# Kernel tuning notes

Measured on AMD Instinct MI355X. Metric: run time of the kernel, lower is better.

The kernel has to match this reference:

```python
import jax, jax.numpy as jnp
import numpy as np

T = 0.07          # temperature
K_POS = 5         # top-k positives per noun and for mask prediction
MARGIN = 0.1
LAM_CONTRAST = 0.6
LAM_MASK = 0.4


def _l2n(x):
    return x / jnp.linalg.norm(x, axis=-1, keepdims=True)


def setup_inputs() -> dict:
    key = jax.random.key(0)
    k0, k1, k2, k3 = jax.random.split(key, 4)
    B, N, D, M = 64, 576, 512, 16  # N = 24*24 patch grid
    patch_feats = _l2n(jax.random.normal(k0, (B, N, D), jnp.float32))
    noun_feats = _l2n(jax.random.normal(k1, (B, M, D), jnp.float32))
    global_img_feat = _l2n(jax.random.normal(k2, (B, D), jnp.float32))
    global_txt_feat = _l2n(jax.random.normal(k3, (B, D), jnp.float32))
    logit_scale = jnp.full((1,), 1.0 / 0.07, jnp.float32)
    idx = jnp.arange(B, dtype=jnp.int32)
    return {
        "patch_feats": patch_feats,
        "noun_feats": noun_feats,
        "global_img_feat": global_img_feat,
        "global_txt_feat": global_txt_feat,
        "logit_scale": logit_scale,
        "idx": idx,
    }


def _fine_grained_loss(patch_feats, noun_feats):
    # sim[b,m,n] = <noun_m, patch_n>; replaces the nested Python loops.
    B = patch_feats.shape[0]
    sim = jnp.einsum('bmd,bnd->bmn', noun_feats, patch_feats)
    scaled = sim / T
    # Per-noun contrastive loss. log_softmax over cat([topk, rest]) equals
    # log_softmax over all N entries evaluated at the topk positions, so:
    #   loss = -sum_topk log_softmax = K_POS*lse - sum(topk scaled values)
    lse = jax.nn.logsumexp(scaled, axis=-1)              # [B, M]
    topv, _ = jax.lax.top_k(scaled, K_POS)               # [B, M, K]
    contrast_loss = jnp.mean(K_POS * lse - topv.sum(-1))
    # Mask-prediction BCE loss (pool_type='mean').
    pooled = sim.mean(axis=1)                            # [B, N]
    _, tidx = jax.lax.top_k(pooled, K_POS)               # [B, K]
    pred = jnp.zeros_like(pooled).at[jnp.arange(B)[:, None], tidx].set(1.0)
    x = pooled / T
    mask_loss = jnp.mean(jnp.logaddexp(0.0, x) - x * pred)
    return LAM_CONTRAST * contrast_loss + LAM_MASK * mask_loss


def _contrastive_loss(img, txt, logit_scale, idx):
    logits = logit_scale.reshape(()) * (img @ txt.T)
    pos = (idx[:, None] == idx[None, :]).astype(logits.dtype)
    labels = pos / pos.sum(axis=1, keepdims=True)
    li2t = -(jax.nn.log_softmax(logits, axis=1) * labels).sum(1).mean()
    lt2i = -(jax.nn.log_softmax(logits.T, axis=1) * labels).sum(1).mean()
    return 0.5 * (li2t + lt2i)


def _triplet_loss(img, txt):
    scores = img @ txt.T
    d = jnp.diagonal(scores)
    eye = jnp.eye(scores.shape[0], dtype=bool)
    cost_s = jnp.where(eye, 0.0, jnp.clip(MARGIN + scores - d[:, None], 0.0)).sum()
    cost_im = jnp.where(eye, 0.0, jnp.clip(MARGIN + scores - d[None, :], 0.0)).sum()
    return 0.5 * (cost_s + cost_im)


def reference(patch_feats, noun_feats, global_img_feat, global_txt_feat, logit_scale, idx):
    loss_c = _contrastive_loss(global_img_feat, global_txt_feat, logit_scale, idx)
    loss_t = _triplet_loss(global_img_feat, global_txt_feat)
    loss_f = _fine_grained_loss(patch_feats, noun_feats)
    return jnp.stack([loss_c, loss_t, loss_f])
```

## Files before the change

### kernel.cpp

```cpp
#include <hip/hip_runtime.h>
#include <hip/hip_bf16.h>
#include <math.h>

#define NB 64
#define NN 576
#define ND 512
#define NM 16
#define QPB 9
#define KPOS 5
#define TINV 14.2857142857142857f

#define NFINE (NB * QPB)
#define NBLK1 (NFINE + NB)
#define WS_SIM 4096

#define FINF __builtin_inff()

typedef __attribute__((ext_vector_type(8))) short short8;
typedef __attribute__((ext_vector_type(4))) float floatx4;

__device__ __forceinline__ short f2bf(float f) {
  unsigned u = __float_as_uint(f);
  u += 0x7FFFu + ((u >> 16) & 1u);
  return (short)(u >> 16);
}

__device__ __forceinline__ short8 pack8(const float4 a, const float4 b) {
  short8 r;
  r[0] = f2bf(a.x); r[1] = f2bf(a.y); r[2] = f2bf(a.z); r[3] = f2bf(a.w);
  r[4] = f2bf(b.x); r[5] = f2bf(b.y); r[6] = f2bf(b.z); r[7] = f2bf(b.w);
  return r;
}

__device__ __forceinline__ void ins5(float (&a)[5], float v) {
  if (v > a[4]) {
    a[4] = v;
    if (a[4] > a[3]) { float x = a[4]; a[4] = a[3]; a[3] = x; }
    if (a[3] > a[2]) { float x = a[3]; a[3] = a[2]; a[2] = x; }
    if (a[2] > a[1]) { float x = a[2]; a[2] = a[1]; a[1] = x; }
    if (a[1] > a[0]) { float x = a[1]; a[1] = a[0]; a[0] = x; }
  }
}

__device__ __forceinline__ void merge5(float (&a)[5], const float (&b)[5]) {
  float r[5];
#pragma unroll
  for (int k = 0; k < 5; ++k) {
    float best = -FINF;
#pragma unroll
    for (int i = 0; i <= k + 1; ++i) {
      const int j = k + 1 - i;
      const float av = (i == 0) ? FINF : a[i - 1];
      const float bv = (j == 0) ? FINF : b[j - 1];
      best = fmaxf(best, fminf(av, bv));
    }
    r[k] = best;
  }
#pragma unroll
  for (int k = 0; k < 5; ++k) a[k] = r[k];
}

__device__ __forceinline__ void merge5_shfl(float (&a)[5], int msk) {
  float o[5];
#pragma unroll
  for (int k = 0; k < 5; ++k) o[k] = __shfl_xor(a[k], msk, 64);
  merge5(a, o);
}

__global__ __launch_bounds__(256) void k_sim(
    const float* __restrict__ patch, const float* __restrict__ noun,
    const float* __restrict__ gimg, const float* __restrict__ gtxt,
    float* __restrict__ ws) {
  const int blk = blockIdx.x;
  const int t = threadIdx.x;
  const int lane = t & 63;

  __shared__ float L[256];

  if (blk < NFINE) {
    const int b = blk / QPB, quad = blk - b * QPB;
    const int w = t >> 6;
    const int nidx = lane & 15;
    const int k0 = (lane >> 4) * 8;

    const float* nrow = noun + ((size_t)b * NM + nidx) * ND + k0;
    const float* prow = patch + ((size_t)(b * NN + quad * 64 + w * 16 + nidx)) * ND + k0;

    floatx4 acc = {0.f, 0.f, 0.f, 0.f};
#pragma unroll
    for (int ks = 0; ks < 16; ++ks) {
      const int o = ks * 32;
      const float4 a0 = *(const float4*)(nrow + o);
      const float4 a1 = *(const float4*)(nrow + o + 4);
      const float4 p0 = *(const float4*)(prow + o);
      const float4 p1 = *(const float4*)(prow + o + 4);
      const short8 af = pack8(a0, a1);
      const short8 bf = pack8(p0, p1);
      acc = __builtin_amdgcn_mfma_f32_16x16x32_bf16(af, bf, acc, 0, 0, 0);
    }

    float* dst = ws + WS_SIM + (size_t)blk * 1024;
    const int mrow = (lane >> 4) * 4;
    const int pcol = w * 16 + nidx;
#pragma unroll
    for (int r = 0; r < 4; ++r) dst[(mrow + r) * 64 + pcol] = acc[r];
  } else {
    const int i = blk - NFINE;
    const int dq = t >> 6;
    const float4* ip = (const float4*)(gimg + (size_t)i * ND + dq * 128);
    const float4* tp = (const float4*)(gtxt + (size_t)lane * ND + dq * 128);
    float a = 0.f;
#pragma unroll
    for (int q = 0; q < 32; ++q) {
      const float4 x = ip[q];
      const float4 y = tp[q];
      a += x.x * y.x + x.y * y.y + x.z * y.z + x.w * y.w;
    }
    L[dq * 64 + lane] = a;
    __syncthreads();
    if (t < 64) ws[i * 64 + t] = L[t] + L[64 + t] + L[128 + t] + L[192 + t];
  }
}

__global__ __launch_bounds__(256) void k_loss(
    const float* __restrict__ ws, const float* __restrict__ lscale,
    const int* __restrict__ idx, float* __restrict__ out) {
  const int blk = blockIdx.x;
  const int t = threadIdx.x;
  const int lane = t & 63;
  const int w = t >> 6;

  __shared__ float S[NM * 577 + 64];

  if (blk < NB) {
    const int b = blk;
#pragma unroll
    for (int q = 0; q < QPB; ++q) {
      const float4* t0 = (const float4*)(ws + WS_SIM + (size_t)(b * QPB + q) * 1024);
      const float4 a = t0[t];
      const int i0 = 4 * t;
      const int m = i0 >> 6, p = i0 & 63;
      float* dst = &S[m * 577 + q * 64 + p];
      dst[0] = a.x * TINV;
      dst[1] = a.y * TINV;
      dst[2] = a.z * TINV;
      dst[3] = a.w * TINV;
    }
    __syncthreads();

    float cpart = 0.f;
#pragma unroll
    for (int mi = 0; mi < 4; ++mi) {
      const int m = w * 4 + mi;
      const float* row = &S[m * 577];
      float mx = -FINF;
#pragma unroll
      for (int k = 0; k < 9; ++k) mx = fmaxf(mx, row[lane + 64 * k]);
#pragma unroll
      for (int msk = 1; msk < 64; msk <<= 1) mx = fmaxf(mx, __shfl_xor(mx, msk, 64));
      float se = 0.f;
      float t5[5] = {-FINF, -FINF, -FINF, -FINF, -FINF};
#pragma unroll
      for (int k = 0; k < 9; ++k) {
        const float v = row[lane + 64 * k];
        se += expf(v - mx);
        ins5(t5, v);
      }
#pragma unroll
      for (int msk = 1; msk < 64; msk <<= 1) {
        se += __shfl_xor(se, msk, 64);
        merge5_shfl(t5, msk);
      }
      if (lane == 0) {
        const float st = t5[0] + t5[1] + t5[2] + t5[3] + t5[4];
        cpart += (KPOS * (mx + logf(se)) - st) * (0.6f / (float)(NB * NM));
      }
    }

    float sxp = 0.f;
    float u5[5] = {-FINF, -FINF, -FINF, -FINF, -FINF};
#pragma unroll
    for (int rep = 0; rep < 3; ++rep) {
      const int n = t + rep * 256;
      if (n < NN) {
        float cs = 0.f;
#pragma unroll
        for (int m = 0; m < NM; ++m) cs += S[m * 577 + n];
        const float x = cs * (1.f / 16.f);
        sxp += (x > 0.f) ? (x + log1pf(expf(-x))) : log1pf(expf(x));
        ins5(u5, x);
      }
    }
#pragma unroll
    for (int msk = 1; msk < 64; msk <<= 1) {
      sxp += __shfl_xor(sxp, msk, 64);
      merge5_shfl(u5, msk);
    }
    float* R = &S[NM * 577];
    if (lane == 0) {
      R[w] = cpart;
      R[8 + w] = sxp;
#pragma unroll
      for (int k = 0; k < 5; ++k) R[16 + w * 5 + k] = u5[k];
    }
    __syncthreads();
    if (t == 0) {
      float tot = R[0] + R[1] + R[2] + R[3];
      float sp = R[8] + R[9] + R[10] + R[11];
      float f5[5] = {R[16], R[17], R[18], R[19], R[20]};
#pragma unroll
      for (int ww = 1; ww < 4; ++ww) {
        float o[5] = {R[16 + ww * 5], R[17 + ww * 5], R[18 + ww * 5],
                      R[19 + ww * 5], R[20 + ww * 5]};
        merge5(f5, o);
      }
      const float st = f5[0] + f5[1] + f5[2] + f5[3] + f5[4];
      tot += (sp - st) * (0.4f / (float)(NB * NN));
      atomicAdd(out + 2, tot);
    }
    return;
  }

  float* S_ = &S[0];
  for (int i = t; i < 4096; i += 256) S_[(i >> 6) * 65 + (i & 63)] = ws[i];
  __syncthreads();
  float* dgp = &S[4160];
  int* idl = (int*)&S[4224];
  if (t < 64) { dgp[t] = S_[t * 66]; idl[t] = idx[t]; }
  __syncthreads();
  if (t < 64) {
    const float sc = lscale[0];
    float mR = -FINF, mC = -FINF;
    for (int j = 0; j < 64; ++j) {
      mR = fmaxf(mR, sc * S_[t * 65 + j]);
      mC = fmaxf(mC, sc * S_[j * 65 + t]);
    }
    float seR = 0.f, seC = 0.f;
    for (int j = 0; j < 64; ++j) {
      seR += expf(sc * S_[t * 65 + j] - mR);
      seC += expf(sc * S_[j * 65 + t] - mC);
    }
    const float lseR = mR + logf(seR);
    const float lseC = mC + logf(seC);
    const int myid = idl[t];
    const float di = dgp[t];
    float ps = 0.f, trow = 0.f, tcol = 0.f, cs = 0.f, ci = 0.f;
    for (int j = 0; j < 64; ++j) {
      const float sv = S_[t * 65 + j];
      const float svT = S_[j * 65 + t];
      if (idl[j] == myid) {
        ps += 1.f;
        trow += sc * sv - lseR;
        tcol += sc * svT - lseC;
      }
      if (j != t) {
        cs += fmaxf(0.f, 0.1f + sv - di);
        ci += fmaxf(0.f, 0.1f + sv - dgp[j]);
      }
    }
    float vc = -(trow + tcol) / ps;
    float vt = cs + ci;
#pragma unroll
    for (int msk = 1; msk < 64; msk <<= 1) {
      vc += __shfl_xor(vc, msk, 64);
      vt += __shfl_xor(vt, msk, 64);
    }
    if (t == 0) {
      out[0] = vc * (0.5f / 64.f);
      out[1] = vt * 0.5f;
    }
  }
}

extern "C" void kernel_launch(void* const* d_in, const int* in_sizes, int n_in,
                              void* d_out, int out_size, void* d_ws, size_t ws_size,
                              hipStream_t stream) {
  const float* patch = (const float*)d_in[0];
  const float* noun  = (const float*)d_in[1];
  const float* gimg  = (const float*)d_in[2];
  const float* gtxt  = (const float*)d_in[3];
  const float* lsc   = (const float*)d_in[4];
  const int*   idx   = (const int*)d_in[5];
  float* out = (float*)d_out;
  float* ws  = (float*)d_ws;

  hipMemsetAsync(d_out, 0, 3 * sizeof(float), stream);
  k_sim<<<dim3(NBLK1), dim3(256), 0, stream>>>(patch, noun, gimg, gtxt, ws);
  k_loss<<<dim3(NB + 1), dim3(256), 0, stream>>>(ws, lsc, idx, out);
}
```

Before: 140.6 us.

## Pre-convert noun features to bf16 in a prep kernel and truncate patch conversion

Adds a small prep kernel that converts noun features to round-to-nearest bf16 in workspace once, so the similarity kernel loads packed bf16 nouns instead of reconverting them in each of 9 blocks per batch. Patch values are now packed to bf16 by plain truncation with a byte-permute instead of rounding, which cuts ALU work but adds truncation error. The MFMA loop is partially unrolled. It adds a kernel launch and slightly changes numerics.

```diff
diff --git a/kernel.cpp b/kernel.cpp
--- a/kernel.cpp
+++ b/kernel.cpp
@@ -13,23 +13,24 @@
 #define NFINE (NB * QPB)
 #define NBLK1 (NFINE + NB)
 #define WS_SIM 4096
+#define WS_NOUNF (WS_SIM + NFINE * 1024)
 
 #define FINF __builtin_inff()
 
 typedef __attribute__((ext_vector_type(8))) short short8;
 typedef __attribute__((ext_vector_type(4))) float floatx4;
 
-__device__ __forceinline__ short f2bf(float f) {
-  unsigned u = __float_as_uint(f);
-  u += 0x7FFFu + ((u >> 16) & 1u);
-  return (short)(u >> 16);
-}
-
-__device__ __forceinline__ short8 pack8(const float4 a, const float4 b) {
-  short8 r;
-  r[0] = f2bf(a.x); r[1] = f2bf(a.y); r[2] = f2bf(a.z); r[3] = f2bf(a.w);
-  r[4] = f2bf(b.x); r[5] = f2bf(b.y); r[6] = f2bf(b.z); r[7] = f2bf(b.w);
-  return r;
+__device__ __forceinline__ unsigned pk2(float lo, float hi) {
+  return __builtin_amdgcn_perm(__float_as_uint(hi), __float_as_uint(lo), 0x07060302u);
+}
+
+__device__ __forceinline__ short8 packB(const float4 a, const float4 b) {
+  union { unsigned u[4]; short8 s; } cv;
+  cv.u[0] = pk2(a.x, a.y);
+  cv.u[1] = pk2(a.z, a.w);
+  cv.u[2] = pk2(b.x, b.y);
+  cv.u[3] = pk2(b.z, b.w);
+  return cv.s;
 }
 
 __device__ __forceinline__ void ins5(float (&a)[5], float v) {
@@ -67,10 +68,25 @@
   merge5(a, o);
 }
 
+__global__ __launch_bounds__(256) void k_prep(
+    const float* __restrict__ noun, float* __restrict__ ws) {
+  const int i = blockIdx.x * 256 + threadIdx.x;
+  const float4 v = ((const float4*)noun)[i];
+  unsigned ux = __float_as_uint(v.x), uy = __float_as_uint(v.y);
+  unsigned uz = __float_as_uint(v.z), uw = __float_as_uint(v.w);
+  ux += 0x7FFFu + ((ux >> 16) & 1u);
+  uy += 0x7FFFu + ((uy >> 16) & 1u);
+  uz += 0x7FFFu + ((uz >> 16) & 1u);
+  uw += 0x7FFFu + ((uw >> 16) & 1u);
+  uint2 o;
+  o.x = __builtin_amdgcn_perm(uy, ux, 0x07060302u);
+  o.y = __builtin_amdgcn_perm(uw, uz, 0x07060302u);
+  ((uint2*)((unsigned short*)(ws + WS_NOUNF)))[i] = o;
+}
+
 __global__ __launch_bounds__(256) void k_sim(
-    const float* __restrict__ patch, const float* __restrict__ noun,
-    const float* __restrict__ gimg, const float* __restrict__ gtxt,
-    float* __restrict__ ws) {
+    const float* __restrict__ patch, const float* __restrict__ gimg,
+    const float* __restrict__ gtxt, float* __restrict__ ws) {
   const int blk = blockIdx.x;
   const int t = threadIdx.x;
   const int lane = t & 63;
@@ -83,19 +99,19 @@
     const int nidx = lane & 15;
     const int k0 = (lane >> 4) * 8;
 
-    const float* nrow = noun + ((size_t)b * NM + nidx) * ND + k0;
-    const float* prow = patch + ((size_t)(b * NN + quad * 64 + w * 16 + nidx)) * ND + k0;
+    const unsigned short* nrow =
+        (const unsigned short*)(ws + WS_NOUNF) + ((size_t)b * NM + nidx) * ND + k0;
+    const float* prow =
+        patch + ((size_t)(b * NN + quad * 64 + w * 16 + nidx)) * ND + k0;
 
     floatx4 acc = {0.f, 0.f, 0.f, 0.f};
-#pragma unroll
+#pragma unroll 4
     for (int ks = 0; ks < 16; ++ks) {
       const int o = ks * 32;
-      const float4 a0 = *(const float4*)(nrow + o);
-      const float4 a1 = *(const float4*)(nrow + o + 4);
+      const short8 af = *(const short8*)(nrow + o);
       const float4 p0 = *(const float4*)(prow + o);
       const float4 p1 = *(const float4*)(prow + o + 4);
-      const short8 af = pack8(a0, a1);
-      const short8 bf = pack8(p0, p1);
+      const short8 bf = packB(p0, p1);
       acc = __builtin_amdgcn_mfma_f32_16x16x32_bf16(af, bf, acc, 0, 0, 0);
     }
 
@@ -285,6 +301,7 @@
   float* ws  = (float*)d_ws;
 
   hipMemsetAsync(d_out, 0, 3 * sizeof(float), stream);
-  k_sim<<<dim3(NBLK1), dim3(256), 0, stream>>>(patch, noun, gimg, gtxt, ws);
+  k_prep<<<dim3(512), dim3(256), 0, stream>>>(noun, ws);
+  k_sim<<<dim3(NBLK1), dim3(256), 0, stream>>>(patch, gimg, gtxt, ws);
   k_loss<<<dim3(NB + 1), dim3(256), 0, stream>>>(ws, lsc, idx, out);
 }
```

Measured after the change: 136.8 us. 1.03x faster.
